# Kernel tuning notes

Hardware: AMD Instinct MI355X
Metric: run time of the kernel (lower is better)

## Reference

```python
import jax, jax.numpy as jnp
import numpy as np

DISTANCE_WEIGHT = 1.001  # self.distence_weight in the torch module


def setup_inputs() -> dict:
    key = jax.random.key(0)
    k1, k2 = jax.random.split(key)
    B, DIM_IN, DIM_OUT = 1024, 512, 512
    x = jax.random.normal(k1, (B, DIM_IN), dtype=jnp.float32)
    centers = jax.random.normal(k2, (DIM_OUT, DIM_IN), dtype=jnp.float32)
    beta = jnp.ones((DIM_OUT,), dtype=jnp.float32)
    return {"x": x, "centers": centers, "beta": beta}


def reference(x, centers, beta):
    # L1 pairwise distance: [B, dim_out]
    sim = jnp.sum(jnp.abs(x[:, None, :] - centers[None, :, :]), axis=-1)
    # negate, shift by global max * distance_weight, scale by beta
    sim = -sim + jnp.max(sim) * DISTANCE_WEIGHT
    return beta * sim
```

## Files before the change

kernel.cpp:

```cpp
#include <hip/hip_runtime.h>


typedef _Float16 h2 __attribute__((ext_vector_type(2)));
typedef float f4 __attribute__((ext_vector_type(4)));
typedef unsigned int u32x4 __attribute__((ext_vector_type(4)));
typedef unsigned int u32x2 __attribute__((ext_vector_type(2)));

#define DIM_O 512
#define DIM_K 512
#define BM 16
#define BN 32
#define BK 64
#define LSTRIDE 36
#define W_DIST 1.001f

__device__ __forceinline__ h2 as_h2(unsigned int u){ h2 r; __builtin_memcpy(&r,&u,4); return r; }
__device__ __forceinline__ unsigned int as_u(h2 h){ unsigned int r; __builtin_memcpy(&r,&h,4); return r; }
__device__ __forceinline__ unsigned int cvt2(float a, float b){
    auto h = __builtin_amdgcn_cvt_pkrtz(a, b);
    unsigned int r; __builtin_memcpy(&r, &h, 4); return r;
}

__global__ __launch_bounds__(64) void k_sim(const float* __restrict__ X,
                                            const float* __restrict__ C,
                                            float* __restrict__ S,
                                            float* __restrict__ bmax)
{
    __shared__ __align__(16) h2 xs[BM][LSTRIDE];
    __shared__ __align__(16) h2 cs[BN][LSTRIDE];
    const int tid = threadIdx.x;
    const int bx = blockIdx.x & 15;
    const int by = blockIdx.x >> 4;
    const int row0 = by * BM, col0 = bx * BN;
    const int tr = tid >> 4;
    const int tc = tid & 15;
    float acc[4][2] = {};
    const h2 one2 = {(_Float16)1.f, (_Float16)1.f};

    f4 xv[4], cv[8];
    const int srow = tid >> 4, skv = tid & 15;
#pragma unroll
    for (int p = 0; p < 4; ++p)
        xv[p] = *(const f4*)(X + (row0 + srow + 4 * p) * DIM_K + 4 * skv);
#pragma unroll
    for (int p = 0; p < 8; ++p)
        cv[p] = *(const f4*)(C + (col0 + srow + 4 * p) * DIM_K + 4 * skv);

    for (int t = 0; t < 8; ++t) {
        __syncthreads();
#pragma unroll
        for (int p = 0; p < 4; ++p) {
            u32x2 w; w[0] = cvt2(xv[p].x, xv[p].y); w[1] = cvt2(xv[p].z, xv[p].w);
            *(u32x2*)&xs[srow + 4 * p][skv * 2] = w;
        }
#pragma unroll
        for (int p = 0; p < 8; ++p) {
            u32x2 w; w[0] = cvt2(cv[p].x, cv[p].y); w[1] = cvt2(cv[p].z, cv[p].w);
            *(u32x2*)&cs[srow + 4 * p][skv * 2] = w;
        }
        __syncthreads();

        const int kn = (t < 7) ? (t + 1) * BK : 0;
#pragma unroll
        for (int p = 0; p < 4; ++p)
            xv[p] = *(const f4*)(X + (row0 + srow + 4 * p) * DIM_K + kn + 4 * skv);
#pragma unroll
        for (int p = 0; p < 8; ++p)
            cv[p] = *(const f4*)(C + (col0 + srow + 4 * p) * DIM_K + kn + 4 * skv);

#pragma unroll
        for (int g = 0; g < 8; ++g) {
            u32x4 xr[4], cr[2];
#pragma unroll
            for (int i = 0; i < 4; ++i)
                xr[i] = *(const u32x4*)&xs[tr * 4 + i][g * 4];
            cr[0] = *(const u32x4*)&cs[tc][g * 4];
            cr[1] = *(const u32x4*)&cs[tc + 16][g * 4];
#pragma unroll
            for (int k2 = 0; k2 < 4; ++k2) {
#pragma unroll
                for (int i = 0; i < 4; ++i) {
                    h2 a = as_h2(xr[i][k2]);
#pragma unroll
                    for (int j = 0; j < 2; ++j) {
                        h2 d = a - as_h2(cr[j][k2]);
                        h2 ad = as_h2(as_u(d) & 0x7fff7fffu);
                        acc[i][j] = __builtin_amdgcn_fdot2(ad, one2, acc[i][j], false);
                    }
                }
            }
        }
    }

    float m = 0.f;
#pragma unroll
    for (int i = 0; i < 4; ++i) {
        const int r = row0 + tr * 4 + i;
        S[r * DIM_O + col0 + tc]      = acc[i][0];
        S[r * DIM_O + col0 + tc + 16] = acc[i][1];
        m = fmaxf(m, fmaxf(acc[i][0], acc[i][1]));
    }
#pragma unroll
    for (int off = 32; off > 0; off >>= 1)
        m = fmaxf(m, __shfl_xor(m, off, 64));
    if (tid == 0) bmax[blockIdx.x] = m;
}

__global__ __launch_bounds__(256) void k_out(float* __restrict__ S,
                                             const float* __restrict__ beta,
                                             const float* __restrict__ bmax)
{
    const int tid = threadIdx.x;
    const int lane = tid & 63;
    float m = 0.f;
#pragma unroll
    for (int i = 0; i < 16; ++i)
        m = fmaxf(m, bmax[lane + 64 * i]);
#pragma unroll
    for (int off = 32; off > 0; off >>= 1)
        m = fmaxf(m, __shfl_xor(m, off, 64));
    const float shift = m * W_DIST;

    const int f = blockIdx.x * 256 + tid;
    f4 s = ((const f4*)S)[f];
    f4 b = ((const f4*)beta)[f & 127];
    f4 r;
    r.x = b.x * (shift - s.x);
    r.y = b.y * (shift - s.y);
    r.z = b.z * (shift - s.z);
    r.w = b.w * (shift - s.w);
    ((f4*)S)[f] = r;
}

extern "C" void kernel_launch(void* const* d_in, const int* in_sizes, int n_in,
                              void* d_out, int out_size, void* d_ws, size_t ws_size,
                              hipStream_t stream) {
    const float* X = (const float*)d_in[0];
    const float* C = (const float*)d_in[1];
    const float* beta = (const float*)d_in[2];
    float* S = (float*)d_out;
    float* bmax = (float*)d_ws;
    k_sim<<<1024, 64, 0, stream>>>(X, C, S, bmax);
    k_out<<<512, 256, 0, stream>>>(S, beta, bmax);
}
```

Baseline: 79.58 us.

## Split-K L1 distance with 64x64 swizzled tiles and separate reduction kernel

Reworks the distance kernel to use 256-thread blocks over 64x64 output tiles, with K split four ways so each block loads its whole 128-wide K slice once into XOR-swizzled shared memory. There is no pipelined K loop anymore. Partial sums go to a workspace buffer, and a new reduction kernel sums the four partials, writes S and computes per-block maxima. This raises per-thread register reuse (4x4 accumulators) and cuts synchronisation. The cost is an extra kernel launch plus about 8 MB of partial-sum traffic through the workspace.

```diff
diff --git a/kernel.cpp b/kernel.cpp
--- a/kernel.cpp
+++ b/kernel.cpp
@@ -4,106 +4,111 @@
 typedef _Float16 h2 __attribute__((ext_vector_type(2)));
 typedef float f4 __attribute__((ext_vector_type(4)));
 typedef unsigned int u32x4 __attribute__((ext_vector_type(4)));
-typedef unsigned int u32x2 __attribute__((ext_vector_type(2)));
 
+#define DIM_K 512
 #define DIM_O 512
-#define DIM_K 512
-#define BM 16
-#define BN 32
-#define BK 64
-#define LSTRIDE 36
+#define NSPLIT 4
+#define KW (DIM_K / NSPLIT)
+#define PSTRIDE (1024 * 512)
 #define W_DIST 1.001f
 
 __device__ __forceinline__ h2 as_h2(unsigned int u){ h2 r; __builtin_memcpy(&r,&u,4); return r; }
-__device__ __forceinline__ unsigned int as_u(h2 h){ unsigned int r; __builtin_memcpy(&r,&h,4); return r; }
 __device__ __forceinline__ unsigned int cvt2(float a, float b){
     auto h = __builtin_amdgcn_cvt_pkrtz(a, b);
     unsigned int r; __builtin_memcpy(&r, &h, 4); return r;
 }
 
-__global__ __launch_bounds__(64) void k_sim(const float* __restrict__ X,
-                                            const float* __restrict__ C,
-                                            float* __restrict__ S,
-                                            float* __restrict__ bmax)
+__global__ __launch_bounds__(256) void k_sim(const float* __restrict__ X,
+                                             const float* __restrict__ C,
+                                             float* __restrict__ P)
 {
-    __shared__ __align__(16) h2 xs[BM][LSTRIDE];
-    __shared__ __align__(16) h2 cs[BN][LSTRIDE];
+    __shared__ __align__(16) unsigned int xs[64 * 64];
+    __shared__ __align__(16) unsigned int cs[64 * 64];
     const int tid = threadIdx.x;
-    const int bx = blockIdx.x & 15;
-    const int by = blockIdx.x >> 4;
-    const int row0 = by * BM, col0 = bx * BN;
-    const int tr = tid >> 4;
+    const int b = blockIdx.x;
+    const int ks = b & 3;
+    const int ct = (b >> 2) & 7;
+    const int rt = b >> 5;
+    const int row0 = rt * 64, col0 = ct * 64, kb = ks * KW;
+
+#pragma unroll
+    for (int p = 0; p < 4; ++p) {
+        const int s = tid + 256 * p;
+        const int row = s >> 4, gI = s & 15, gg = gI ^ (row & 7);
+        const float* xg = X + (row0 + row) * DIM_K + kb + gg * 8;
+        f4 a = *(const f4*)xg; f4 bb = *(const f4*)(xg + 4);
+        u32x4 w; w[0]=cvt2(a.x,a.y); w[1]=cvt2(a.z,a.w); w[2]=cvt2(bb.x,bb.y); w[3]=cvt2(bb.z,bb.w);
+        *(u32x4*)&xs[row * 64 + gI * 4] = w;
+        const float* cg = C + (col0 + row) * DIM_K + kb + gg * 8;
+        a = *(const f4*)cg; bb = *(const f4*)(cg + 4);
+        u32x4 v; v[0]=cvt2(a.x,a.y); v[1]=cvt2(a.z,a.w); v[2]=cvt2(bb.x,bb.y); v[3]=cvt2(bb.z,bb.w);
+        *(u32x4*)&cs[row * 64 + gI * 4] = v;
+    }
+    __syncthreads();
+
+    const int rb = (tid >> 4) * 4;
     const int tc = tid & 15;
-    float acc[4][2] = {};
+    float acc[4][4] = {};
     const h2 one2 = {(_Float16)1.f, (_Float16)1.f};
 
-    f4 xv[4], cv[8];
-    const int srow = tid >> 4, skv = tid & 15;
 #pragma unroll
-    for (int p = 0; p < 4; ++p)
-        xv[p] = *(const f4*)(X + (row0 + srow + 4 * p) * DIM_K + 4 * skv);
+    for (int g = 0; g < 16; ++g) {
+        u32x4 xr[4], cr[4];
 #pragma unroll
-    for (int p = 0; p < 8; ++p)
-        cv[p] = *(const f4*)(C + (col0 + srow + 4 * p) * DIM_K + 4 * skv);
-
-    for (int t = 0; t < 8; ++t) {
-        __syncthreads();
-#pragma unroll
-        for (int p = 0; p < 4; ++p) {
-            u32x2 w; w[0] = cvt2(xv[p].x, xv[p].y); w[1] = cvt2(xv[p].z, xv[p].w);
-            *(u32x2*)&xs[srow + 4 * p][skv * 2] = w;
+        for (int i = 0; i < 4; ++i) {
+            const int r = rb + i;
+            xr[i] = *(const u32x4*)&xs[r * 64 + (g ^ (r & 7)) * 4];
         }
 #pragma unroll
-        for (int p = 0; p < 8; ++p) {
-            u32x2 w; w[0] = cvt2(cv[p].x, cv[p].y); w[1] = cvt2(cv[p].z, cv[p].w);
-            *(u32x2*)&cs[srow + 4 * p][skv * 2] = w;
+        for (int j = 0; j < 4; ++j) {
+            const int c = tc + 16 * j;
+            cr[j] = *(const u32x4*)&cs[c * 64 + (g ^ (c & 7)) * 4];
         }
-        __syncthreads();
-
-        const int kn = (t < 7) ? (t + 1) * BK : 0;
 #pragma unroll
-        for (int p = 0; p < 4; ++p)
-            xv[p] = *(const f4*)(X + (row0 + srow + 4 * p) * DIM_K + kn + 4 * skv);
+        for (int k2 = 0; k2 < 4; ++k2) {
 #pragma unroll
-        for (int p = 0; p < 8; ++p)
-            cv[p] = *(const f4*)(C + (col0 + srow + 4 * p) * DIM_K + kn + 4 * skv);
-
+            for (int i = 0; i < 4; ++i) {
+                const h2 a = as_h2(xr[i][k2]);
 #pragma unroll
-        for (int g = 0; g < 8; ++g) {
-            u32x4 xr[4], cr[2];
-#pragma unroll
-            for (int i = 0; i < 4; ++i)
-                xr[i] = *(const u32x4*)&xs[tr * 4 + i][g * 4];
-            cr[0] = *(const u32x4*)&cs[tc][g * 4];
-            cr[1] = *(const u32x4*)&cs[tc + 16][g * 4];
-#pragma unroll
-            for (int k2 = 0; k2 < 4; ++k2) {
-#pragma unroll
-                for (int i = 0; i < 4; ++i) {
-                    h2 a = as_h2(xr[i][k2]);
-#pragma unroll
-                    for (int j = 0; j < 2; ++j) {
-                        h2 d = a - as_h2(cr[j][k2]);
-                        h2 ad = as_h2(as_u(d) & 0x7fff7fffu);
-                        acc[i][j] = __builtin_amdgcn_fdot2(ad, one2, acc[i][j], false);
-                    }
+                for (int j = 0; j < 4; ++j) {
+                    h2 d = a - as_h2(cr[j][k2]);
+                    unsigned int du; __builtin_memcpy(&du, &d, 4);
+                    h2 ad = as_h2(du & 0x7fff7fffu);
+                    acc[i][j] = __builtin_amdgcn_fdot2(ad, one2, acc[i][j], false);
                 }
             }
         }
     }
 
-    float m = 0.f;
+    float* Pk = P + ks * PSTRIDE;
 #pragma unroll
     for (int i = 0; i < 4; ++i) {
-        const int r = row0 + tr * 4 + i;
-        S[r * DIM_O + col0 + tc]      = acc[i][0];
-        S[r * DIM_O + col0 + tc + 16] = acc[i][1];
-        m = fmaxf(m, fmaxf(acc[i][0], acc[i][1]));
+        const int row = row0 + rb + i;
+#pragma unroll
+        for (int j = 0; j < 4; ++j)
+            Pk[row * DIM_O + col0 + tc + 16 * j] = acc[i][j];
     }
+}
+
+__global__ __launch_bounds__(256) void k_red(const float* __restrict__ P,
+                                             float* __restrict__ S,
+                                             float* __restrict__ bmax)
+{
+    const int tid = threadIdx.x;
+    const int f = blockIdx.x * 256 + tid;
+    const f4* P4 = (const f4*)P;
+    const int q = PSTRIDE / 4;
+    f4 s = P4[f] + P4[f + q] + P4[f + 2 * q] + P4[f + 3 * q];
+    ((f4*)S)[f] = s;
+    float m = fmaxf(fmaxf(s.x, s.y), fmaxf(s.z, s.w));
 #pragma unroll
     for (int off = 32; off > 0; off >>= 1)
         m = fmaxf(m, __shfl_xor(m, off, 64));
-    if (tid == 0) bmax[blockIdx.x] = m;
+    __shared__ float wm[4];
+    if ((tid & 63) == 0) wm[tid >> 6] = m;
+    __syncthreads();
+    if (tid == 0)
+        bmax[blockIdx.x] = fmaxf(fmaxf(wm[0], wm[1]), fmaxf(wm[2], wm[3]));
 }
 
 __global__ __launch_bounds__(256) void k_out(float* __restrict__ S,
@@ -114,7 +119,7 @@
     const int lane = tid & 63;
     float m = 0.f;
 #pragma unroll
-    for (int i = 0; i < 16; ++i)
+    for (int i = 0; i < 8; ++i)
         m = fmaxf(m, bmax[lane + 64 * i]);
 #pragma unroll
     for (int off = 32; off > 0; off >>= 1)
@@ -139,7 +144,9 @@
     const float* C = (const float*)d_in[1];
     const float* beta = (const float*)d_in[2];
     float* S = (float*)d_out;
-    float* bmax = (float*)d_ws;
-    k_sim<<<1024, 64, 0, stream>>>(X, C, S, bmax);
+    float* P = (float*)d_ws;
+    float* bmax = (float*)d_ws + NSPLIT * PSTRIDE;
+    k_sim<<<512, 256, 0, stream>>>(X, C, P);
+    k_red<<<512, 256, 0, stream>>>(P, S, bmax);
     k_out<<<512, 256, 0, stream>>>(S, beta, bmax);
 }
```

Measured after the change: 79.62 us. About the same (+0.1%).
